# Kernel tuning notes

Hardware: AMD Instinct MI355X
Metric: run time of the kernel (lower is better)

Reference implementation:

```python
import jax, jax.numpy as jnp
import numpy as np

H = 256      # HIDDEN_DIM
F_IN = 16    # input_dim
B = 512
S = 168      # encoder sequence length
T = 24       # PRED_LEN


def _lstm_cell(x, h, c, w_ih, w_hh, b):
    # torch gate order: i, f, g, o
    g = x @ w_ih.T + h @ w_hh.T + b
    i, f, gg, o = jnp.split(g, 4, axis=-1)
    c_new = jax.nn.sigmoid(f) * c + jax.nn.sigmoid(i) * jnp.tanh(gg)
    h_new = jax.nn.sigmoid(o) * jnp.tanh(c_new)
    return h_new, c_new


def _lstm_layer(x, w_ih, w_hh, b):
    # x: [S, B, in] -> outputs [S, B, H], final (h, c)
    Bv, Hv = x.shape[1], w_hh.shape[1]
    init = (jnp.zeros((Bv, Hv), x.dtype), jnp.zeros((Bv, Hv), x.dtype))
    def step(carry, xt):
        h, c = _lstm_cell(xt, carry[0], carry[1], w_ih, w_hh, b)
        return (h, c), h
    (h, c), ys = jax.lax.scan(step, init, x)
    return ys, h, c


def setup_inputs() -> dict:
    key = jax.random.key(0)
    ks = jax.random.split(key, 24)
    s = 1.0 / np.sqrt(H)
    u = lambda k, shape: jax.random.uniform(k, shape, jnp.float32, -s, s)
    inp = {}
    inp['src'] = jax.random.normal(ks[0], (B, S, F_IN), jnp.float32)
    # encoder LSTM (2 layers); biases b_ih + b_hh fused into one vector
    inp['enc_w_ih0'] = u(ks[1], (4 * H, F_IN))
    inp['enc_w_hh0'] = u(ks[2], (4 * H, H))
    inp['enc_b0'] = u(ks[3], (4 * H,))
    inp['enc_w_ih1'] = u(ks[4], (4 * H, H))
    inp['enc_w_hh1'] = u(ks[5], (4 * H, H))
    inp['enc_b1'] = u(ks[6], (4 * H,))
    # decoder LSTM (2 layers), input_size = 1 + H
    inp['dec_w_ih0'] = u(ks[7], (4 * H, 1 + H))
    inp['dec_w_hh0'] = u(ks[8], (4 * H, H))
    inp['dec_b0'] = u(ks[9], (4 * H,))
    inp['dec_w_ih1'] = u(ks[10], (4 * H, H))
    inp['dec_w_hh1'] = u(ks[11], (4 * H, H))
    inp['dec_b1'] = u(ks[12], (4 * H,))
    # attention: Linear(2H -> H), v: Linear(H -> 1, no bias), position bias
    inp['attn_w'] = u(ks[13], (H, 2 * H))
    inp['attn_b'] = u(ks[14], (H,))
    inp['attn_v'] = u(ks[15], (H,))
    inp['pos_bias'] = jax.random.normal(ks[16], (H,), jnp.float32)
    # fc_out: Linear(H -> 1)
    inp['fc_w'] = u(ks[17], (1, H))
    inp['fc_b'] = u(ks[18], (1,))
    return inp


def reference(src, enc_w_ih0, enc_w_hh0, enc_b0, enc_w_ih1, enc_w_hh1, enc_b1,
              dec_w_ih0, dec_w_hh0, dec_b0, dec_w_ih1, dec_w_hh1, dec_b1,
              attn_w, attn_b, attn_v, pos_bias, fc_w, fc_b):
    x = jnp.transpose(src, (1, 0, 2))  # [S, B, F]
    y0, _, _ = _lstm_layer(x, enc_w_ih0, enc_w_hh0, enc_b0)
    enc_out_t, h1e, c1e = _lstm_layer(y0, enc_w_ih1, enc_w_hh1, enc_b1)
    # also need final state of layer 0 for decoder init
    h0e, c0e = y0[-1], None
    # recompute layer-0 final cell state: rerun scan carry output
    # (cheap alternative: _lstm_layer returns (ys, h, c); reuse it)
    _, h0e, c0e = _lstm_layer(x, enc_w_ih0, enc_w_hh0, enc_b0)
    enc_out = jnp.transpose(enc_out_t, (1, 0, 2))  # [B, S, H]

    We, Wd = attn_w[:, :H], attn_w[:, H:]
    enc_proj = jnp.einsum('bsh,gh->bsg', enc_out, We)  # precomputed encoder projection
    dec_in0 = src[:, -1, -1:]  # [B, 1]

    def dec_step(carry, t):
        h0, c0, h1, c1, dec_in = carry
        # additive attention using top-layer decoder hidden
        e = jnp.tanh(enc_proj + (h1 @ Wd.T + attn_b)[:, None, :])
        e = e + pos_bias[None, None, :] * (t / 24.0)
        w = jax.nn.softmax(e @ attn_v, axis=1)              # [B, S]
        ctx = jnp.einsum('bs,bsh->bh', w, enc_out)          # [B, H]
        x0 = jnp.concatenate([dec_in, ctx], axis=1)          # [B, 1+H]
        h0n, c0n = _lstm_cell(x0, h0, c0, dec_w_ih0, dec_w_hh0, dec_b0)
        h1n, c1n = _lstm_cell(h0n, h1, c1, dec_w_ih1, dec_w_hh1, dec_b1)
        pred = h1n @ fc_w.T + fc_b                           # [B, 1]
        # NOTE: the gated blend of decoder_output in the source is dead code
        # (the blended tensor is never used), so it is omitted here.
        return (h0n, c0n, h1n, c1n, pred), pred

    ts = jnp.arange(T, dtype=src.dtype)
    _, preds = jax.lax.scan(dec_step, (h0e, c0e, h1e, c1e, dec_in0), ts)
    return jnp.transpose(preds, (1, 0, 2))  # [B, T, 1]
```

## Files before the change

### kernel.cpp

```cpp
#include <hip/hip_runtime.h>
#include <hip/hip_fp16.h>
#include <math.h>

#define BB 512
#define HH 256
#define SS 168
#define TT 24
#define NBLK 256
#define NTHR 256
typedef unsigned long long ull;
typedef unsigned short u16;
#define BH 131072ull

#define O_Y0  0ull
#define O_H1  262144ull
#define O_H0  524288ull
#define O_CTX 786432ull
#define O_W0  933888ull
#define O_W1  1261568ull
#define O_WP  2834432ull
#define O_WDT 2835456ull
#define O_BP  2900992ull
#define O_E16 2905088ull
#define O_P16 13915136ull

typedef float f32x4 __attribute__((ext_vector_type(4)));
typedef float v2f __attribute__((ext_vector_type(2)));
typedef unsigned int ru4 __attribute__((ext_vector_type(4)));

__device__ __forceinline__ float sigf(float x) { return 1.f / (1.f + expf(-x)); }

#define AR __ATOMIC_RELAXED
#define SCA __HIP_MEMORY_SCOPE_AGENT
__device__ __forceinline__ int aLd(int* p) { return __hip_atomic_load(p, AR, SCA); }
__device__ __forceinline__ int aAdd(int* p, int v) { return __hip_atomic_fetch_add(p, v, AR, SCA); }

__device__ __forceinline__ float2 ld2(const float* p) {
  ull raw = __hip_atomic_load((const ull*)p, AR, SCA);
  float2 v; v.x = __uint_as_float((unsigned)raw); v.y = __uint_as_float((unsigned)(raw >> 32));
  return v;
}
__device__ __forceinline__ float ld1(const float* p) {
  unsigned raw = __hip_atomic_load((const unsigned*)p, AR, SCA);
  return __uint_as_float(raw);
}
__device__ __forceinline__ void st1(float* p, float v) {
  __hip_atomic_store((unsigned*)p, __float_as_uint(v), AR, SCA);
}
__device__ __forceinline__ void sth(__half* p, __half v) {
  __hip_atomic_store((unsigned short*)p, __half_as_ushort(v), AR, SCA);
}
__device__ __forceinline__ void stu(unsigned* p, unsigned v) {
  __hip_atomic_store(p, v, AR, SCA);
}

__device__ __forceinline__ void ld_h(const float* p, v2f& a, v2f& b) {
  asm volatile("global_load_dwordx2 %0, %2, off sc0 sc1\n\t"
               "global_load_dwordx2 %1, %3, off sc0 sc1"
               : "=&v"(a), "=&v"(b) : "v"(p), "v"(p + 16) : "memory");
}
struct W4 { ru4 v[4]; };
__device__ __forceinline__ void ld_w4(const u16* ph, const u16* pl, W4& w) {
  asm volatile("global_load_dwordx4 %0, %4, off\n\t"
               "global_load_dwordx4 %1, %5, off\n\t"
               "global_load_dwordx4 %2, %6, off\n\t"
               "global_load_dwordx4 %3, %7, off"
               : "=&v"(w.v[0]), "=&v"(w.v[1]), "=&v"(w.v[2]), "=&v"(w.v[3])
               : "v"(ph), "v"(ph + 8), "v"(pl), "v"(pl + 8) : "memory");
}
#define VMW(n) asm volatile("s_waitcnt vmcnt(" #n ")" ::: "memory")

#define MFMA(d, a, b) asm volatile("v_mfma_f32_16x16x32_bf16 %0, %1, %2, %0" \
                                   : "+v"(d) : "v"(a), "v"(b))
#define TOUCH(x) asm volatile("" : "+v"(x))

__device__ __forceinline__ void poll(int* f, int tgt) {
  while (aLd(f) < tgt) __builtin_amdgcn_s_sleep(1);
}
__device__ __forceinline__ void flag_arrive(int* f) {
  asm volatile("s_waitcnt vmcnt(0)" ::: "memory");
  __syncthreads();
  if (threadIdx.x == 0) aAdd(f, 1);
}
__device__ __forceinline__ void flag_wait2(int* f0, int t0, int* f1, int t1) {
  if (threadIdx.x == 0 && f0) poll(f0, t0);
  if (threadIdx.x == 64 && f1) poll(f1, t1);
  __syncthreads();
}

struct SMT {
  union {
    struct { unsigned WsH[128][20]; unsigned WsL[128][20]; float Hs[32][36]; } m;
    struct { float As[32][65];  float Bs[32][65]; } g;
    struct { float h1s[256], qs[256], vs[256], sc[192], ctxs[512], sred[4]; } at;
  };
};

__device__ __forceinline__ void fma16(float acc[4][4], const float4 hv, const float4 wv) {
  acc[0][0] += hv.x * wv.x; acc[0][1] += hv.x * wv.y; acc[0][2] += hv.x * wv.z; acc[0][3] += hv.x * wv.w;
  acc[1][0] += hv.y * wv.x; acc[1][1] += hv.y * wv.y; acc[1][2] += hv.y * wv.z; acc[1][3] += hv.y * wv.w;
  acc[2][0] += hv.z * wv.x; acc[2][1] += hv.z * wv.y; acc[2][2] += hv.z * wv.z; acc[2][3] += hv.z * wv.w;
  acc[3][0] += hv.w * wv.x; acc[3][1] += hv.w * wv.y; acc[3][2] += hv.w * wv.z; acc[3][3] += hv.w * wv.w;
}

__device__ __forceinline__ unsigned rne16(unsigned u) {
  return (u + 0x7fffu + ((u >> 16) & 1u)) >> 16;
}
__device__ __forceinline__ void split8s(const float* v8, ru4& hi, ru4& lo) {
#pragma unroll
  for (int j = 0; j < 4; j++) {
    const float a = v8[2 * j], b = v8[2 * j + 1];
    const unsigned ha = rne16(__float_as_uint(a)), hb = rne16(__float_as_uint(b));
    const float ra = a - __uint_as_float(ha << 16);
    const float rb = b - __uint_as_float(hb << 16);
    hi[j] = (ha & 0xffffu) | (hb << 16);
    lo[j] = (rne16(__float_as_uint(ra)) & 0xffffu) | (rne16(__float_as_uint(rb)) << 16);
  }
}

__device__ __forceinline__ void comp_mfma(SMT& sm, int wq, int w1, int l15, int l4,
                                          f32x4 acc[4])
{
  const int hr = w1 * 16 + l15;
  float v8[8];
#pragma unroll
  for (int j = 0; j < 8; j++) v8[j] = sm.m.Hs[l4 * 8 + j][hr];
  ru4 bhi, blo;
  split8s(v8, bhi, blo);
  asm volatile("s_nop 1" : "+v"(bhi), "+v"(blo));
#pragma unroll
  for (int g = 0; g < 4; g++) {
    const int cr = wq * 64 + g * 16 + l15;
    ru4 ah = *(const ru4*)&sm.m.WsH[cr][l4 * 4];
    ru4 al = *(const ru4*)&sm.m.WsL[cr][l4 * 4];
    MFMA(acc[g], ah, bhi);
    MFMA(acc[g], ah, blo);
    MFMA(acc[g], al, bhi);
  }
}

__device__ void gemm_pipe(const u16* wbh, const u16* wbl,
                          const float* hb0, const float* hb1,
                          int NC, int nc0, f32x4 acc[4], SMT& sm,
                          int wq, int w1, int l15, int l4)
{
  const int tid = threadIdx.x;
  const int r = tid & 31, p2 = tid >> 5;
  const int cgt = tid & 127, kt = tid >> 7;
  v2f hA0, hA1, hB0, hB1;
  W4 wA, wB;
  const float* h1p = hb1 - (ull)nc0 * 32;
  ld_h(hb0, hA0, hA1);
  ld_w4(wbh, wbl, wA);
  for (int c = 0; c < NC; c += 2) {
    ld_w4(wbh + (c + 1) * 32, wbl + (c + 1) * 32, wB);
    ld_h((c + 1 < nc0 ? hb0 + (c + 1) * 32 : h1p + (c + 1) * 32), hB0, hB1);
    VMW(6);
    *(ru4*)&sm.m.WsH[cgt][kt * 8]     = wA.v[0];
    *(ru4*)&sm.m.WsH[cgt][kt * 8 + 4] = wA.v[1];
    *(ru4*)&sm.m.WsL[cgt][kt * 8]     = wA.v[2];
    *(ru4*)&sm.m.WsL[cgt][kt * 8 + 4] = wA.v[3];
    sm.m.Hs[p2 * 2][r] = hA0[0]; sm.m.Hs[p2 * 2 + 1][r] = hA0[1];
    sm.m.Hs[(p2 + 8) * 2][r] = hA1[0]; sm.m.Hs[(p2 + 8) * 2 + 1][r] = hA1[1];
    __syncthreads();
    comp_mfma(sm, wq, w1, l15, l4, acc);
    __syncthreads();
    ld_w4(wbh + (c + 2) * 32, wbl + (c + 2) * 32, wA);
    ld_h((c + 2 < nc0 ? hb0 + (c + 2) * 32 : h1p + (c + 2) * 32), hA0, hA1);
    VMW(6);
    *(ru4*)&sm.m.WsH[cgt][kt * 8]     = wB.v[0];
    *(ru4*)&sm.m.WsH[cgt][kt * 8 + 4] = wB.v[1];
    *(ru4*)&sm.m.WsL[cgt][kt * 8]     = wB.v[2];
    *(ru4*)&sm.m.WsL[cgt][kt * 8 + 4] = wB.v[3];
    sm.m.Hs[p2 * 2][r] = hB0[0]; sm.m.Hs[p2 * 2 + 1][r] = hB0[1];
    sm.m.Hs[(p2 + 8) * 2][r] = hB1[0]; sm.m.Hs[(p2 + 8) * 2 + 1][r] = hB1[1];
    __syncthreads();
    comp_mfma(sm, wq, w1, l15, l4, acc);
    __syncthreads();
  }
  asm volatile("s_waitcnt vmcnt(0)" ::: "memory");
  asm volatile("s_nop 7\n\ts_nop 7"
               : "+v"(acc[0]), "+v"(acc[1]), "+v"(acc[2]), "+v"(acc[3]));
}

__device__ __forceinline__ void lstm_epi4(f32x4 acc[4], float cR[4], int row, int ubase, int l4,
                                          float* hout, __half* e16, int sstep)
{
#pragma unroll
  for (int g = 0; g < 4; g++) {
    const int u = ubase + g * 4 + l4;
    const float iv = sigf(acc[g][0]), fv = sigf(acc[g][1]);
    const float gv = tanhf(acc[g][2]), ov = sigf(acc[g][3]);
    const float cn = fv * cR[g] + iv * gv;
    cR[g] = cn;
    const float hn = ov * tanhf(cn);
    st1(hout + (ull)row * 256 + u, hn);
    if (e16) sth(e16 + ((ull)row * SS + sstep) * 256 + u, __float2half(hn));
  }
}

__device__ void attn_fc(int row, int t, int slot, const float* h1r, const float* wdT,
                        const float* attn_b, const float* attn_v,
                        const __half* P16, const __half* E16,
                        const float* fc_w, const float* fc_b,
                        float* ctxb, float* out, SMT& sm)
{
  const int tid = threadIdx.x;
  __syncthreads();
  if (tid < 128) {
    float2 v = ld2(h1r + (ull)slot * BH + (ull)row * 256 + tid * 2);
    sm.at.h1s[tid * 2] = v.x; sm.at.h1s[tid * 2 + 1] = v.y;
  }
  __syncthreads();
  if (t >= 1 && tid < 64) {
    float a = 0.f;
#pragma unroll
    for (int j = 0; j < 4; j++) a += sm.at.h1s[tid + 64 * j] * fc_w[tid + 64 * j];
#pragma unroll
    for (int m = 32; m >= 1; m >>= 1) a += __shfl_xor(a, m, 64);
    if (tid == 0) {
      const float p = a + fc_b[0];
      out[(ull)row * TT + (t - 1)] = p;
      st1(ctxb + (ull)row * 288 + 256, p);
    }
  }
  if (t >= TT) return;
  float qv = attn_b[tid];
  for (int k = 0; k < 256; k += 4) {
    qv += sm.at.h1s[k]     * wdT[(ull)(k)     * 256 + tid];
    qv += sm.at.h1s[k + 1] * wdT[(ull)(k + 1) * 256 + tid];
    qv += sm.at.h1s[k + 2] * wdT[(ull)(k + 2) * 256 + tid];
    qv += sm.at.h1s[k + 3] * wdT[(ull)(k + 3) * 256 + tid];
  }
  sm.at.qs[tid] = qv;
  sm.at.vs[tid] = attn_v[tid];
  __syncthreads();
  const int wv = tid >> 6, lane = tid & 63;
  for (int s = wv; s < SS; s += 4) {
    const __half2* Pr = (const __half2*)(P16 + ((ull)row * SS + s) * 256);
    float a = 0.f;
#pragma unroll
    for (int jj = 0; jj < 2; jj++) {
      const int i2 = lane + 64 * jj;
      const float2 pv = __half22float2(Pr[i2]);
      const int g0 = i2 * 2;
      a += sm.at.vs[g0] * tanhf(pv.x + sm.at.qs[g0]);
      a += sm.at.vs[g0 + 1] * tanhf(pv.y + sm.at.qs[g0 + 1]);
    }
#pragma unroll
    for (int m = 32; m >= 1; m >>= 1) a += __shfl_xor(a, m, 64);
    if (lane == 0) sm.at.sc[s] = a;
  }
  __syncthreads();
  if (tid < 64) {
    float m = -1e30f;
    for (int i = tid; i < SS; i += 64) m = fmaxf(m, sm.at.sc[i]);
#pragma unroll
    for (int mm = 32; mm >= 1; mm >>= 1) m = fmaxf(m, __shfl_xor(m, mm, 64));
    if (tid == 0) sm.at.sred[0] = m;
  }
  __syncthreads();
  const float smax = sm.at.sred[0];
  if (tid < SS) sm.at.sc[tid] = expf(sm.at.sc[tid] - smax);
  __syncthreads();
  if (tid < 64) {
    float ssum = 0.f;
    for (int i = tid; i < SS; i += 64) ssum += sm.at.sc[i];
#pragma unroll
    for (int mm = 32; mm >= 1; mm >>= 1) ssum += __shfl_xor(ssum, mm, 64);
    if (tid == 0) sm.at.sred[1] = ssum;
  }
  __syncthreads();
  const float rinv = 1.f / sm.at.sred[1];
  const int u2 = tid & 127, sh = tid >> 7;
  float cx = 0.f, cy = 0.f;
  for (int s = sh * 84; s < sh * 84 + 84; s++) {
    const float w = sm.at.sc[s] * rinv;
    const float2 ev = __half22float2(*(const __half2*)(E16 + ((ull)row * SS + s) * 256 + u2 * 2));
    cx += w * ev.x; cy += w * ev.y;
  }
  sm.at.ctxs[sh * 256 + u2 * 2] = cx;
  sm.at.ctxs[sh * 256 + u2 * 2 + 1] = cy;
  __syncthreads();
  st1(ctxb + (ull)row * 288 + tid, sm.at.ctxs[tid] + sm.at.ctxs[256 + tid]);
}

__device__ void proj_tile(const __half* E16, const float* attn_w, __half* P16,
                          int m0, int n0, SMT& sm)
{
  const int tid = threadIdx.x;
  const int mq = tid & 15, nq = tid >> 4;
  const int li = tid & 63, kq = tid >> 6;
  float acc[4][4] = {{0.f}};
  for (int k0 = 0; k0 < 256; k0 += 32) {
    float4 raw = *(const float4*)(E16 + (ull)(m0 + li) * 256 + k0 + kq * 8);
    const __half* hp = (const __half*)&raw;
#pragma unroll
    for (int i = 0; i < 8; i++) sm.g.As[kq * 8 + i][li] = __half2float(hp[i]);
    const float* gb = attn_w + (ull)(n0 + li) * 512 + k0 + kq * 8;
    const float4 v0 = *(const float4*)gb, v1 = *(const float4*)(gb + 4);
    sm.g.Bs[kq * 8 + 0][li] = v0.x; sm.g.Bs[kq * 8 + 1][li] = v0.y;
    sm.g.Bs[kq * 8 + 2][li] = v0.z; sm.g.Bs[kq * 8 + 3][li] = v0.w;
    sm.g.Bs[kq * 8 + 4][li] = v1.x; sm.g.Bs[kq * 8 + 5][li] = v1.y;
    sm.g.Bs[kq * 8 + 6][li] = v1.z; sm.g.Bs[kq * 8 + 7][li] = v1.w;
    __syncthreads();
#pragma unroll 8
    for (int kk = 0; kk < 32; kk++) {
      const float4 a4 = *(const float4*)&sm.g.As[kk][mq * 4];
      const float4 b4 = *(const float4*)&sm.g.Bs[kk][nq * 4];
      fma16(acc, a4, b4);
    }
    __syncthreads();
  }
#pragma unroll
  for (int i = 0; i < 4; i++) {
    const int m = m0 + mq * 4 + i;
#pragma unroll
    for (int j = 0; j < 2; j++) {
      __half2 h2; h2.x = __float2half(acc[i][j * 2]); h2.y = __float2half(acc[i][j * 2 + 1]);
      stu((unsigned*)(P16 + (ull)m * 256 + n0 + nq * 4) + j, *(unsigned*)&h2);
    }
  }
}

__global__ __launch_bounds__(256, 1) void seq2seq_pipe(
    const float* __restrict__ src,
    const float* __restrict__ attn_w, const float* __restrict__ attn_b,
    const float* __restrict__ attn_v,
    const float* __restrict__ fc_w, const float* __restrict__ fc_b,
    float* __restrict__ out, int* __restrict__ ib)
{
  __shared__ SMT sm;
  const int blk = blockIdx.x;
  const int tid = threadIdx.x;
  float* fb = (float*)ib + 65536;
  float* y0r  = fb + O_Y0;
  float* h1r  = fb + O_H1;
  float* h0r  = fb + O_H0;
  float* zb   = h0r + BH;
  float* ctxb = fb + O_CTX;
  const u16* whi0 = (const u16*)(fb + O_W0);
  const u16* wlo0 = whi0 + 1024ull * 320;
  const u16* whi1 = (const u16*)(fb + O_W1);
  const u16* wlo1 = whi1 + 1024ull * 512;
  const u16* dhi0 = whi1 + 2ull * 1024 * 512;
  const u16* dlo0 = whi1 + 3ull * 1024 * 512;
  const u16* dhi1 = whi1 + 4ull * 1024 * 512;
  const u16* dlo1 = whi1 + 5ull * 1024 * 512;
  const float* wp  = fb + O_WP;
  const float* wdT = fb + O_WDT;
  const float* bp  = fb + O_BP;
  __half* E16 = (__half*)(fb + O_E16);
  __half* P16 = (__half*)(fb + O_P16);
  const int g = blk >> 5, m = blk & 31;
  const int rowg = g * 64;
  int* gf = ib + g * 1024;
  int* ife = gf;
  int* ifa = gf + 704; int* ifh0 = gf + 736; int* ifh1 = gf + 768; int* ifp = gf + 900;

  const int lm = (m < 16) ? m : (m - 16);
  const int row0 = rowg + (lm & 1) * 32;
  const int gc0 = (lm >> 1) * 128;
  const int w = tid >> 6;
  const int l15 = tid & 15, l4 = (tid >> 4) & 3;
  const int wq = w >> 1, w1 = w & 1;
  const int gcw = gc0 + wq * 64;
  const int myrow = row0 + w1 * 16 + l15;
  const int ubase = gcw >> 2;
  const int r = tid & 31;
  const int cgt = tid & 127, kt = tid >> 7;

  float cReg[4] = {0.f, 0.f, 0.f, 0.f};

  for (int t = 0; t <= SS; t++) {
    flag_wait2(t ? ife + (t - 1) : nullptr, 32, nullptr, 0);
    if (m < 16) {
      if (t < SS) {
        f32x4 acc[4];
#pragma unroll
        for (int gg = 0; gg < 4; gg++) {
          acc[gg] = *(const f32x4*)(bp + gcw + gg * 16 + l4 * 4);
          TOUCH(acc[gg]);
        }
        {
          W4 wx;
          ld_w4(whi0 + (ull)(gc0 + cgt) * 320 + kt * 16,
                wlo0 + (ull)(gc0 + cgt) * 320 + kt * 16, wx);
          VMW(0);
          *(ru4*)&sm.m.WsH[cgt][kt * 8]     = wx.v[0];
          *(ru4*)&sm.m.WsH[cgt][kt * 8 + 4] = wx.v[1];
          *(ru4*)&sm.m.WsL[cgt][kt * 8]     = wx.v[2];
          *(ru4*)&sm.m.WsL[cgt][kt * 8 + 4] = wx.v[3];
          const int f = tid >> 5;
          sm.m.Hs[f][r]      = src[((ull)(row0 + r) * SS + t) * 16 + f];
          sm.m.Hs[f + 8][r]  = src[((ull)(row0 + r) * SS + t) * 16 + f + 8];
          sm.m.Hs[f + 16][r] = 0.f;
          sm.m.Hs[f + 24][r] = 0.f;
          __syncthreads();
          comp_mfma(sm, wq, w1, l15, l4, acc);
          __syncthreads();
        }
        const float* ysrc = (t == 0) ? zb : (y0r + (ull)((t + 1) & 1) * BH);
        const float* hb0 = ysrc + (ull)(row0 + r) * 256 + (tid >> 5) * 2;
        gemm_pipe(whi0 + (ull)(gc0 + cgt) * 320 + 32 + kt * 16,
                  wlo0 + (ull)(gc0 + cgt) * 320 + 32 + kt * 16,
                  hb0, hb0, 8, 8, acc, sm, wq, w1, l15, l4);
        lstm_epi4(acc, cReg, myrow, ubase, l4, y0r + (ull)(t & 1) * BH, nullptr, 0);
      }
    } else {
      if (t >= 1) {
        const int s = t - 1;
        f32x4 acc[4];
#pragma unroll
        for (int gg = 0; gg < 4; gg++) {
          acc[gg] = *(const f32x4*)(bp + 1024 + gcw + gg * 16 + l4 * 4);
          TOUCH(acc[gg]);
        }
        const float* ysrc = y0r + (ull)(s & 1) * BH;
        const float* hsrc = (s == 0) ? zb : (h1r + (ull)((s + 1) & 1) * BH);
        const float* hb0 = ysrc + (ull)(row0 + r) * 256 + (tid >> 5) * 2;
        const float* hb1 = hsrc + (ull)(row0 + r) * 256 + (tid >> 5) * 2;
        gemm_pipe(whi1 + (ull)(gc0 + cgt) * 512 + kt * 16,
                  wlo1 + (ull)(gc0 + cgt) * 512 + kt * 16,
                  hb0, hb1, 16, 8, acc, sm, wq, w1, l15, l4);
        lstm_epi4(acc, cReg, myrow, ubase, l4, h1r + (ull)(s & 1) * BH, E16, s);
      }
    }
    flag_arrive(ife + t);
  }

  if (tid == 0) poll(ife + SS, 32);
  __syncthreads();
  {
    const int em0 = rowg * SS;
    for (int tau = m; tau < 672; tau += 32)
      proj_tile(E16, attn_w, P16, em0 + (tau >> 2) * 64, (tau & 3) * 64, sm);
  }
  flag_arrive(ifp);

  for (int t = 0; t <= TT; t++) {
    if (t == 0) flag_wait2(ifp, 32, nullptr, 0);
    else flag_wait2(ifh1 + (t - 1), 16, nullptr, 0);
    const int slot = (t + 1) & 1;
    attn_fc(rowg + 2 * m,     t, slot, h1r, wdT, attn_b, attn_v, P16, E16, fc_w, fc_b, ctxb, out, sm);
    attn_fc(rowg + 2 * m + 1, t, slot, h1r, wdT, attn_b, attn_v, P16, E16, fc_w, fc_b, ctxb, out, sm);
    if (t == TT) break;
    flag_arrive(ifa + t);
    if (m < 16) {
      flag_wait2(ifa + t, 32, t ? ifh0 + (t - 1) : nullptr, 16);
      f32x4 acc[4];
#pragma unroll
      for (int gg = 0; gg < 4; gg++) {
        acc[gg] = *(const f32x4*)(bp + 2048 + gcw + gg * 16 + l4 * 4);
        TOUCH(acc[gg]);
      }
      const float* h0src = (t == 0) ? (y0r + BH) : (h0r + (ull)((t + 1) & 1) * BH);
      const float* hb0 = ctxb + (ull)(row0 + r) * 288 + (tid >> 5) * 2;
      const float* hb1 = h0src + (ull)(row0 + r) * 256 + (tid >> 5) * 2;
      gemm_pipe(dhi0 + (ull)(gc0 + cgt) * 512 + kt * 16,
                dlo0 + (ull)(gc0 + cgt) * 512 + kt * 16,
                hb0, hb1, 16, 8, acc, sm, wq, w1, l15, l4);
      const float p = ld1(ctxb + (ull)myrow * 288 + 256);
#pragma unroll
      for (int gg = 0; gg < 4; gg++) {
        const f32x4 wpv = *(const f32x4*)(wp + gcw + gg * 16 + l4 * 4);
        acc[gg] = acc[gg] + wpv * p;
      }
      lstm_epi4(acc, cReg, myrow, ubase, l4, h0r + (ull)(t & 1) * BH, nullptr, 0);
      flag_arrive(ifh0 + t);
    } else {
      flag_wait2(ifh0 + t, 16, t ? ifh1 + (t - 1) : nullptr, 16);
      f32x4 acc[4];
#pragma unroll
      for (int gg = 0; gg < 4; gg++) {
        acc[gg] = *(const f32x4*)(bp + 3072 + gcw + gg * 16 + l4 * 4);
        TOUCH(acc[gg]);
      }
      const float* hb0 = h0r + (ull)(t & 1) * BH + (ull)(row0 + r) * 256 + (tid >> 5) * 2;
      const float* hb1 = h1r + (ull)((t + 1) & 1) * BH + (ull)(row0 + r) * 256 + (tid >> 5) * 2;
      gemm_pipe(dhi1 + (ull)(gc0 + cgt) * 512 + kt * 16,
                dlo1 + (ull)(gc0 + cgt) * 512 + kt * 16,
                hb0, hb1, 16, 8, acc, sm, wq, w1, l15, l4);
      lstm_epi4(acc, cReg, myrow, ubase, l4, h1r + (ull)(t & 1) * BH, nullptr, 0);
      flag_arrive(ifh1 + t);
    }
  }
}

__device__ __forceinline__ void split_store(float v, u16* hi, u16* lo, ull i) {
  const unsigned u = __float_as_uint(v);
  const unsigned hb = (u + 0x7fffu + ((u >> 16) & 1u)) >> 16;
  const float rr = v - __uint_as_float(hb << 16);
  const unsigned ur = __float_as_uint(rr);
  const unsigned lb = (ur + 0x7fffu + ((ur >> 16) & 1u)) >> 16;
  hi[i] = (u16)hb; lo[i] = (u16)lb;
}

__global__ void init_all(
    const float* __restrict__ src,
    const float* __restrict__ ewih0, const float* __restrict__ ewhh0, const float* __restrict__ eb0,
    const float* __restrict__ ewih1, const float* __restrict__ ewhh1, const float* __restrict__ eb1,
    const float* __restrict__ dwih0, const float* __restrict__ dwhh0, const float* __restrict__ db0,
    const float* __restrict__ dwih1, const float* __restrict__ dwhh1, const float* __restrict__ db1,
    const float* __restrict__ attn_w, int* __restrict__ ib)
{
  const int gid = blockIdx.x * 256 + threadIdx.x;
  const int NG = 1024 * 256;
  float* fb = (float*)ib + 65536;
  u16* whi0 = (u16*)(fb + O_W0);
  u16* wlo0 = whi0 + 1024ull * 320;
  u16* whi1 = (u16*)(fb + O_W1);
  u16* wlo1 = whi1 + 1024ull * 512;
  u16* dhi0 = whi1 + 2ull * 1024 * 512;
  u16* dlo0 = whi1 + 3ull * 1024 * 512;
  u16* dhi1 = whi1 + 4ull * 1024 * 512;
  u16* dlo1 = whi1 + 5ull * 1024 * 512;
  float* wpd = fb + O_WP;

  for (int i = gid; i < 8192; i += NG) ib[i] = 0;
  for (int i = gid; i < (int)BH; i += NG) fb[O_H0 + BH + i] = 0.f;
  for (int i = gid; i < 1024 * 320; i += NG) {
    const int cg = i / 320, k = i - cg * 320, j = (cg & 3) * 256 + (cg >> 2);
    float v = 0.f;
    if (k < 16) v = ewih0[(ull)j * 16 + k];
    else if (k >= 32 && k < 288) v = ewhh0[(ull)j * 256 + (k - 32)];
    split_store(v, whi0, wlo0, i);
  }
  for (int i = gid; i < 1024 * 512; i += NG) {
    const int cg = i >> 9, k = i & 511, j = (cg & 3) * 256 + (cg >> 2);
    split_store((k < 256) ? ewih1[(ull)j * 256 + k] : ewhh1[(ull)j * 256 + k - 256], whi1, wlo1, i);
    split_store((k < 256) ? dwih0[(ull)j * 257 + 1 + k] : dwhh0[(ull)j * 256 + k - 256], dhi0, dlo0, i);
    split_store((k < 256) ? dwih1[(ull)j * 256 + k] : dwhh1[(ull)j * 256 + k - 256], dhi1, dlo1, i);
  }
  for (int i = gid; i < 1024; i += NG) {
    const int j = (i & 3) * 256 + (i >> 2);
    wpd[i] = dwih0[(ull)j * 257];
  }
  for (int i = gid; i < 256 * 256; i += NG) {
    const int k = i >> 8, gg = i & 255;
    fb[O_WDT + i] = attn_w[(ull)gg * 512 + 256 + k];
  }
  for (int i = gid; i < 4096; i += NG) {
    const int set = i >> 10, cg = i & 1023, j = (cg & 3) * 256 + (cg >> 2);
    const float* bsrc = (set == 0) ? eb0 : (set == 1) ? eb1 : (set == 2) ? db0 : db1;
    fb[O_BP + i] = bsrc[j];
  }
  for (int i = gid; i < 512; i += NG)
    fb[O_CTX + (ull)i * 288 + 256] = src[((ull)i * SS + 167) * 16 + 15];
}

extern "C" void kernel_launch(void* const* d_in, const int* in_sizes, int n_in,
                              void* d_out, int out_size, void* d_ws, size_t ws_size,
                              hipStream_t stream)
{
  const float* src    = (const float*)d_in[0];
  const float* ewih0  = (const float*)d_in[1];
  const float* ewhh0  = (const float*)d_in[2];
  const float* eb0    = (const float*)d_in[3];
  const float* ewih1  = (const float*)d_in[4];
  const float* ewhh1  = (const float*)d_in[5];
  const float* eb1    = (const float*)d_in[6];
  const float* dwih0  = (const float*)d_in[7];
  const float* dwhh0  = (const float*)d_in[8];
  const float* db0    = (const float*)d_in[9];
  const float* dwih1  = (const float*)d_in[10];
  const float* dwhh1  = (const float*)d_in[11];
  const float* db1    = (const float*)d_in[12];
  const float* attn_w = (const float*)d_in[13];
  const float* attn_b = (const float*)d_in[14];
  const float* attn_v = (const float*)d_in[15];
  const float* fc_w   = (const float*)d_in[17];
  const float* fc_b   = (const float*)d_in[18];
  float* out = (float*)d_out;
  int* ib    = (int*)d_ws;

  init_all<<<1024, 256, 0, stream>>>(src, ewih0, ewhh0, eb0, ewih1, ewhh1, eb1,
                                     dwih0, dwhh0, db0, dwih1, dwhh1, db1, attn_w, ib);

  void* args[] = {
    (void*)&src, (void*)&attn_w, (void*)&attn_b, (void*)&attn_v,
    (void*)&fc_w, (void*)&fc_b, (void*)&out, (void*)&ib,
  };
  hipError_t lerr = hipLaunchCooperativeKernel((const void*)seq2seq_pipe, dim3(NBLK), dim3(NTHR),
                                               args, 0, stream);
  if (lerr != hipSuccess) {
    hipLaunchKernelGGL(seq2seq_pipe, dim3(NBLK), dim3(NTHR), 0, stream,
                       src, attn_w, attn_b, attn_v, fc_w, fc_b, out, ib);
  }
}
```

Measured before the change: 7.700 ms.

## Deepen GEMM prefetch pipeline and transpose H tile for vector LDS reads

The hidden-state tile in shared memory is transposed so each lane reads its eight K values with two 128-bit LDS loads instead of eight scalar loads. The gemm_pipe loop is restructured into a four-stage register rotation that issues loads two to three chunks ahead and places them after the barrier, overlapping global latency with MFMA work. This costs more registers, which may reduce occupancy. The loop now assumes NC is a multiple of four and prefetches past the end.

```diff
diff --git a/kernel.cpp b/kernel.cpp
--- a/kernel.cpp
+++ b/kernel.cpp
@@ -90,7 +90,7 @@
 
 struct SMT {
   union {
-    struct { unsigned WsH[128][20]; unsigned WsL[128][20]; float Hs[32][36]; } m;
+    struct { unsigned WsH[128][20]; unsigned WsL[128][20]; float Ht[32][36]; } m;
     struct { float As[32][65];  float Bs[32][65]; } g;
     struct { float h1s[256], qs[256], vs[256], sc[192], ctxs[512], sred[4]; } at;
   };
@@ -106,15 +106,16 @@
 __device__ __forceinline__ unsigned rne16(unsigned u) {
   return (u + 0x7fffu + ((u >> 16) & 1u)) >> 16;
 }
-__device__ __forceinline__ void split8s(const float* v8, ru4& hi, ru4& lo) {
+__device__ __forceinline__ void split8v(const f32x4 a, const f32x4 b, ru4& hi, ru4& lo) {
 #pragma unroll
   for (int j = 0; j < 4; j++) {
-    const float a = v8[2 * j], b = v8[2 * j + 1];
-    const unsigned ha = rne16(__float_as_uint(a)), hb = rne16(__float_as_uint(b));
-    const float ra = a - __uint_as_float(ha << 16);
-    const float rb = b - __uint_as_float(hb << 16);
-    hi[j] = (ha & 0xffffu) | (hb << 16);
-    lo[j] = (rne16(__float_as_uint(ra)) & 0xffffu) | (rne16(__float_as_uint(rb)) << 16);
+    const float x = (j < 2) ? a[2 * j] : b[2 * j - 4];
+    const float y = (j < 2) ? a[2 * j + 1] : b[2 * j - 3];
+    const unsigned hx = rne16(__float_as_uint(x)), hy = rne16(__float_as_uint(y));
+    const float rx = x - __uint_as_float(hx << 16);
+    const float ry = y - __uint_as_float(hy << 16);
+    hi[j] = (hx & 0xffffu) | (hy << 16);
+    lo[j] = (rne16(__float_as_uint(rx)) & 0xffffu) | (rne16(__float_as_uint(ry)) << 16);
   }
 }
 
@@ -122,11 +123,10 @@
                                           f32x4 acc[4])
 {
   const int hr = w1 * 16 + l15;
-  float v8[8];
-#pragma unroll
-  for (int j = 0; j < 8; j++) v8[j] = sm.m.Hs[l4 * 8 + j][hr];
+  const f32x4 hv0 = *(const f32x4*)&sm.m.Ht[hr][l4 * 8];
+  const f32x4 hv1 = *(const f32x4*)&sm.m.Ht[hr][l4 * 8 + 4];
   ru4 bhi, blo;
-  split8s(v8, bhi, blo);
+  split8v(hv0, hv1, bhi, blo);
   asm volatile("s_nop 1" : "+v"(bhi), "+v"(blo));
 #pragma unroll
   for (int g = 0; g < 4; g++) {
@@ -139,6 +139,15 @@
   }
 }
 
+#define STW(wv) do { \
+  *(ru4*)&sm.m.WsH[cgt][kt * 8]     = (wv).v[0]; \
+  *(ru4*)&sm.m.WsH[cgt][kt * 8 + 4] = (wv).v[1]; \
+  *(ru4*)&sm.m.WsL[cgt][kt * 8]     = (wv).v[2]; \
+  *(ru4*)&sm.m.WsL[cgt][kt * 8 + 4] = (wv).v[3]; } while (0)
+#define STH(a, b) do { \
+  sm.m.Ht[r][p2 * 2]      = (a)[0]; sm.m.Ht[r][p2 * 2 + 1]  = (a)[1]; \
+  sm.m.Ht[r][p2 * 2 + 16] = (b)[0]; sm.m.Ht[r][p2 * 2 + 17] = (b)[1]; } while (0)
+
 __device__ void gemm_pipe(const u16* wbh, const u16* wbl,
                           const float* hb0, const float* hb1,
                           int NC, int nc0, f32x4 acc[4], SMT& sm,
@@ -147,40 +156,49 @@
   const int tid = threadIdx.x;
   const int r = tid & 31, p2 = tid >> 5;
   const int cgt = tid & 127, kt = tid >> 7;
-  v2f hA0, hA1, hB0, hB1;
-  W4 wA, wB;
   const float* h1p = hb1 - (ull)nc0 * 32;
-  ld_h(hb0, hA0, hA1);
-  ld_w4(wbh, wbl, wA);
-  for (int c = 0; c < NC; c += 2) {
-    ld_w4(wbh + (c + 1) * 32, wbl + (c + 1) * 32, wB);
-    ld_h((c + 1 < nc0 ? hb0 + (c + 1) * 32 : h1p + (c + 1) * 32), hB0, hB1);
-    VMW(6);
-    *(ru4*)&sm.m.WsH[cgt][kt * 8]     = wA.v[0];
-    *(ru4*)&sm.m.WsH[cgt][kt * 8 + 4] = wA.v[1];
-    *(ru4*)&sm.m.WsL[cgt][kt * 8]     = wA.v[2];
-    *(ru4*)&sm.m.WsL[cgt][kt * 8 + 4] = wA.v[3];
-    sm.m.Hs[p2 * 2][r] = hA0[0]; sm.m.Hs[p2 * 2 + 1][r] = hA0[1];
-    sm.m.Hs[(p2 + 8) * 2][r] = hA1[0]; sm.m.Hs[(p2 + 8) * 2 + 1][r] = hA1[1];
-    __syncthreads();
+#define HBk(k) (((k) < nc0) ? (hb0 + (k) * 32) : (h1p + (k) * 32))
+  W4 wr0, wr1, wr2, wr3;
+  v2f h0a, h0b, h1a, h1b, h2a, h2b, h3a, h3b;
+  ld_w4(wbh, wbl, wr0);
+  ld_h(HBk(0), h0a, h0b);
+  ld_w4(wbh + 32, wbl + 32, wr1);
+  ld_h(HBk(1), h1a, h1b);
+  ld_h(HBk(2), h2a, h2b);
+  for (int c = 0; c < NC; c += 4) {
+    VMW(8);
+    STW(wr0); STH(h0a, h0b);
+    __syncthreads();
+    ld_w4(wbh + (c + 2) * 32, wbl + (c + 2) * 32, wr2);
+    ld_h(HBk(c + 3), h3a, h3b);
     comp_mfma(sm, wq, w1, l15, l4, acc);
     __syncthreads();
-    ld_w4(wbh + (c + 2) * 32, wbl + (c + 2) * 32, wA);
-    ld_h((c + 2 < nc0 ? hb0 + (c + 2) * 32 : h1p + (c + 2) * 32), hA0, hA1);
-    VMW(6);
-    *(ru4*)&sm.m.WsH[cgt][kt * 8]     = wB.v[0];
-    *(ru4*)&sm.m.WsH[cgt][kt * 8 + 4] = wB.v[1];
-    *(ru4*)&sm.m.WsL[cgt][kt * 8]     = wB.v[2];
-    *(ru4*)&sm.m.WsL[cgt][kt * 8 + 4] = wB.v[3];
-    sm.m.Hs[p2 * 2][r] = hB0[0]; sm.m.Hs[p2 * 2 + 1][r] = hB0[1];
-    sm.m.Hs[(p2 + 8) * 2][r] = hB1[0]; sm.m.Hs[(p2 + 8) * 2 + 1][r] = hB1[1];
-    __syncthreads();
+    VMW(8);
+    STW(wr1); STH(h1a, h1b);
+    __syncthreads();
+    ld_w4(wbh + (c + 3) * 32, wbl + (c + 3) * 32, wr3);
+    ld_h(HBk(c + 4), h0a, h0b);
+    comp_mfma(sm, wq, w1, l15, l4, acc);
+    __syncthreads();
+    VMW(8);
+    STW(wr2); STH(h2a, h2b);
+    __syncthreads();
+    ld_w4(wbh + (c + 4) * 32, wbl + (c + 4) * 32, wr0);
+    ld_h(HBk(c + 5), h1a, h1b);
+    comp_mfma(sm, wq, w1, l15, l4, acc);
+    __syncthreads();
+    VMW(8);
+    STW(wr3); STH(h3a, h3b);
+    __syncthreads();
+    ld_w4(wbh + (c + 5) * 32, wbl + (c + 5) * 32, wr1);
+    ld_h(HBk(c + 6), h2a, h2b);
     comp_mfma(sm, wq, w1, l15, l4, acc);
     __syncthreads();
   }
   asm volatile("s_waitcnt vmcnt(0)" ::: "memory");
   asm volatile("s_nop 7\n\ts_nop 7"
                : "+v"(acc[0]), "+v"(acc[1]), "+v"(acc[2]), "+v"(acc[3]));
+#undef HBk
 }
 
 __device__ __forceinline__ void lstm_epi4(f32x4 acc[4], float cR[4], int row, int ubase, int l4,
@@ -392,10 +410,10 @@
           *(ru4*)&sm.m.WsL[cgt][kt * 8]     = wx.v[2];
           *(ru4*)&sm.m.WsL[cgt][kt * 8 + 4] = wx.v[3];
           const int f = tid >> 5;
-          sm.m.Hs[f][r]      = src[((ull)(row0 + r) * SS + t) * 16 + f];
-          sm.m.Hs[f + 8][r]  = src[((ull)(row0 + r) * SS + t) * 16 + f + 8];
-          sm.m.Hs[f + 16][r] = 0.f;
-          sm.m.Hs[f + 24][r] = 0.f;
+          sm.m.Ht[r][f]      = src[((ull)(row0 + r) * SS + t) * 16 + f];
+          sm.m.Ht[r][f + 8]  = src[((ull)(row0 + r) * SS + t) * 16 + f + 8];
+          sm.m.Ht[r][f + 16] = 0.f;
+          sm.m.Ht[r][f + 24] = 0.f;
           __syncthreads();
           comp_mfma(sm, wq, w1, l15, l4, acc);
           __syncthreads();
```

New measurement: 7.867 ms. 1.02x slower.
